# Kernel optimization log

Measured on AMD Instinct MI355X. Metric: run time of the kernel, lower is better.

The kernel has to match this reference:

```python
import jax, jax.numpy as jnp
import numpy as np


def setup_inputs() -> dict:
    key = jax.random.key(0)
    ks = jax.random.split(key, 5)
    B, S, D, H, dk = 4, 2048, 1024, 16, 64
    s = 0.02
    return {
        "x": jax.random.normal(ks[0], (B, S, D), dtype=jnp.float32),
        "Wq": jax.random.normal(ks[1], (H, D, dk), dtype=jnp.float32) * s,
        "Wk": jax.random.normal(ks[2], (H, D, dk), dtype=jnp.float32) * s,
        "Wv": jax.random.normal(ks[3], (H, D, dk), dtype=jnp.float32) * s,
        "Wo": jax.random.normal(ks[4], (H * dk, D), dtype=jnp.float32) * s,
    }


def reference(x, Wq, Wk, Wv, Wo):
    # Per-head projections: [B,S,D] x [H,D,dk] -> [B,H,S,dk]
    Q = jnp.einsum("bsd,hdk->bhsk", x, Wq)
    K = jnp.einsum("bsd,hdk->bhsk", x, Wk)
    V = jnp.einsum("bsd,hdk->bhsk", x, Wv)
    scale = 1.0 / jnp.sqrt(jnp.asarray(Wq.shape[-1], x.dtype))
    scores = jnp.einsum("bhqk,bhsk->bhqs", Q, K) * scale  # [B,H,S,S]
    attn = jax.nn.softmax(scores, axis=-1)
    out = jnp.einsum("bhqs,bhsk->bhqk", attn, V)  # [B,H,S,dk]
    B, H, S, dk = out.shape
    # concat heads along feature dim (matches torch.cat over head outputs)
    out = out.transpose(0, 2, 1, 3).reshape(B, S, H * dk)
    return out @ Wo  # [B,S,D]
```

## Files before the change

kernel.cpp:

```cpp
#include <hip/hip_runtime.h>
#include <hip/hip_bf16.h>
#include <stdint.h>

typedef __attribute__((ext_vector_type(8))) short bf16x8;
typedef __attribute__((ext_vector_type(4))) float f32x4;
typedef __attribute__((ext_vector_type(4))) unsigned short us4;

#define AS1C(p) ((const __attribute__((address_space(1))) void*)(p))
#define AS3(p)  ((__attribute__((address_space(3))) void*)(p))

#if __has_builtin(__builtin_amdgcn_exp2f)
#define EXP2(x) __builtin_amdgcn_exp2f(x)
#else
#define EXP2(x) __expf((x) * 0.69314718f)
#endif

#define MAX3(a,b,c) fmaxf(fmaxf((a),(b)),(c))

static __device__ __forceinline__ unsigned short f2b(float f) {
  union { __hip_bfloat16 h; unsigned short u; } cv;
  cv.h = __float2bfloat16(f);
  return cv.u;
}

static __device__ __forceinline__ unsigned int cvtpk(float a, float b) {
  unsigned int r;
  asm("v_cvt_pk_bf16_f32 %0, %1, %2" : "=v"(r) : "v"(a), "v"(b));
  return r;
}

__global__ __launch_bounds__(256) void conv_x_kernel(const float* __restrict__ x,
                                                     unsigned short* __restrict__ xb,
                                                     int n4) {
  int i = blockIdx.x * 256 + threadIdx.x;
  if (i >= n4) return;
  float4 v = ((const float4*)x)[i];
  us4 r = { f2b(v.x), f2b(v.y), f2b(v.z), f2b(v.w) };
  *(us4*)&xb[(size_t)i * 4] = r;
}

__global__ __launch_bounds__(256) void conv_wqkv_kernel(const float* __restrict__ Wq,
                                                        const float* __restrict__ Wk,
                                                        const float* __restrict__ Wv,
                                                        unsigned short* __restrict__ WqkvT) {
  int bid = blockIdx.x;
  int which = bid >> 8;
  int h  = (bid >> 4) & 15;
  int dt = bid & 15;
  const float* W = (which == 0) ? Wq : (which == 1 ? Wk : Wv);
  __shared__ float tile[64][65];
  const int t = threadIdx.x;
  const int c  = t & 63;
  const int r0 = t >> 6;
  const float* src = W + (size_t)h * 65536 + (size_t)dt * 64 * 64;
#pragma unroll
  for (int it = 0; it < 16; ++it) {
    int r = r0 + it * 4;
    tile[r][c] = src[r * 64 + c];
  }
  __syncthreads();
  const size_t n0 = (size_t)which * 1024 + h * 64;
  const int d0 = dt * 64;
#pragma unroll
  for (int it = 0; it < 16; ++it) {
    int cc = r0 + it * 4;
    WqkvT[(n0 + cc) * 1024 + d0 + c] = f2b(tile[c][cc]);
  }
}

__global__ __launch_bounds__(256) void conv_wo_kernel(const float* __restrict__ Wo,
                                                      unsigned short* __restrict__ WoT) {
  int kt = blockIdx.x >> 4, nt = blockIdx.x & 15;
  __shared__ float tile[64][65];
  const int t = threadIdx.x;
  const int c  = t & 63;
  const int r0 = t >> 6;
  const float* src = Wo + (size_t)(kt * 64) * 1024 + nt * 64;
#pragma unroll
  for (int it = 0; it < 16; ++it) {
    int r = r0 + it * 4;
    tile[r][c] = src[(size_t)r * 1024 + c];
  }
  __syncthreads();
#pragma unroll
  for (int it = 0; it < 16; ++it) {
    int cc = r0 + it * 4;
    WoT[((size_t)nt * 64 + cc) * 1024 + kt * 64 + c] = f2b(tile[c][cc]);
  }
}

__global__ __launch_bounds__(256) void gemm_qkv_kernel(
    const unsigned short* __restrict__ A,
    const unsigned short* __restrict__ Bt,
    unsigned short* __restrict__ Q,
    unsigned short* __restrict__ Ko,
    unsigned short* __restrict__ Vt) {
  __shared__ __align__(16) unsigned short sA[128 * 32];
  __shared__ __align__(16) unsigned short sB[128 * 32];
  const int tid  = threadIdx.x;
  const int lane = tid & 63;
  const int wid  = tid >> 6;
  const int wr = wid >> 1, wc = wid & 1;
  const int n0 = blockIdx.y * 24 + blockIdx.x;
  const int n1 = (n0 & 7) * 192 + (n0 >> 3);
  const int brow = (n1 / 24) * 128;
  const int bcol = (n1 % 24) * 128;
  const int K = 1024;

  f32x4 acc[4][4] = {};

  const int r4 = tid >> 2;
  const int c8 = (tid & 3) * 8;
  const unsigned short* ga = A  + (size_t)(brow + r4) * K + c8;
  const unsigned short* gb = Bt + (size_t)(bcol + r4) * K + c8;
  unsigned short* lAw = sA + wid * 512;
  unsigned short* lBw = sB + wid * 512;

  for (int kb = 0; kb < K; kb += 32) {
    if (kb) __syncthreads();
    __builtin_amdgcn_global_load_lds(AS1C(ga + kb),            AS3(lAw),        16, 0, 0);
    __builtin_amdgcn_global_load_lds(AS1C(ga + 64 * K + kb),   AS3(lAw + 2048), 16, 0, 0);
    __builtin_amdgcn_global_load_lds(AS1C(gb + kb),            AS3(lBw),        16, 0, 0);
    __builtin_amdgcn_global_load_lds(AS1C(gb + 64 * K + kb),   AS3(lBw + 2048), 16, 0, 0);
    __syncthreads();

    bf16x8 af[4], bfr[4];
#pragma unroll
    for (int mi = 0; mi < 4; ++mi)
      af[mi] = *(const bf16x8*)&sA[(wr * 64 + mi * 16 + (lane & 15)) * 32 + (lane >> 4) * 8];
#pragma unroll
    for (int ni = 0; ni < 4; ++ni)
      bfr[ni] = *(const bf16x8*)&sB[(wc * 64 + ni * 16 + (lane & 15)) * 32 + (lane >> 4) * 8];
#pragma unroll
    for (int mi = 0; mi < 4; ++mi)
#pragma unroll
      for (int ni = 0; ni < 4; ++ni)
        acc[mi][ni] = __builtin_amdgcn_mfma_f32_16x16x32_bf16(af[mi], bfr[ni], acc[mi][ni], 0, 0, 0);
  }

#pragma unroll
  for (int mi = 0; mi < 4; ++mi) {
    int row0 = brow + wr * 64 + mi * 16 + (lane >> 4) * 4;
    int b = row0 >> 11, s0 = row0 & 2047;
#pragma unroll
    for (int ni = 0; ni < 4; ++ni) {
      int col = bcol + wc * 64 + ni * 16 + (lane & 15);
      int which = col >> 10;
      int h  = (col >> 6) & 15;
      int kk = col & 63;
      if (which == 2) {
        us4 pk = { f2b(acc[mi][ni][0]), f2b(acc[mi][ni][1]),
                   f2b(acc[mi][ni][2]), f2b(acc[mi][ni][3]) };
        *(us4*)&Vt[((size_t)(b * 16 + h) * 64 + kk) * 2048 + s0] = pk;
      } else {
        unsigned short* dst = (which == 0) ? Q : Ko;
        float scl = (which == 0) ? 0.18033688f : 1.0f;
#pragma unroll
        for (int j = 0; j < 4; ++j)
          dst[((size_t)(b * 16 + h) * 2048 + (s0 + j)) * 64 + kk] = f2b(acc[mi][ni][j] * scl);
      }
    }
  }
}

__global__ __launch_bounds__(256) void gemm_out_kernel(
    const unsigned short* __restrict__ A,
    const unsigned short* __restrict__ Bt,
    float* __restrict__ out) {
  __shared__ __align__(16) unsigned short sA[128 * 32];
  __shared__ __align__(16) unsigned short sB[128 * 32];
  const int tid  = threadIdx.x;
  const int lane = tid & 63;
  const int wid  = tid >> 6;
  const int wr = wid >> 1, wc = wid & 1;
  const int n0 = blockIdx.y * 8 + blockIdx.x;
  const int n1 = (n0 & 7) * 64 + (n0 >> 3);
  const int brow = (n1 >> 3) * 128;
  const int bcol = (n1 & 7) * 128;
  const int K = 1024;

  f32x4 acc[4][4] = {};

  const int r4 = tid >> 2;
  const int c8 = (tid & 3) * 8;
  const unsigned short* ga = A  + (size_t)(brow + r4) * K + c8;
  const unsigned short* gb = Bt + (size_t)(bcol + r4) * K + c8;
  unsigned short* lAw = sA + wid * 512;
  unsigned short* lBw = sB + wid * 512;

  for (int kb = 0; kb < K; kb += 32) {
    if (kb) __syncthreads();
    __builtin_amdgcn_global_load_lds(AS1C(ga + kb),          AS3(lAw),        16, 0, 0);
    __builtin_amdgcn_global_load_lds(AS1C(ga + 64 * K + kb), AS3(lAw + 2048), 16, 0, 0);
    __builtin_amdgcn_global_load_lds(AS1C(gb + kb),          AS3(lBw),        16, 0, 0);
    __builtin_amdgcn_global_load_lds(AS1C(gb + 64 * K + kb), AS3(lBw + 2048), 16, 0, 0);
    __syncthreads();

    bf16x8 af[4], bfr[4];
#pragma unroll
    for (int mi = 0; mi < 4; ++mi)
      af[mi] = *(const bf16x8*)&sA[(wr * 64 + mi * 16 + (lane & 15)) * 32 + (lane >> 4) * 8];
#pragma unroll
    for (int ni = 0; ni < 4; ++ni)
      bfr[ni] = *(const bf16x8*)&sB[(wc * 64 + ni * 16 + (lane & 15)) * 32 + (lane >> 4) * 8];
#pragma unroll
    for (int mi = 0; mi < 4; ++mi)
#pragma unroll
      for (int ni = 0; ni < 4; ++ni)
        acc[mi][ni] = __builtin_amdgcn_mfma_f32_16x16x32_bf16(af[mi], bfr[ni], acc[mi][ni], 0, 0, 0);
  }

#pragma unroll
  for (int mi = 0; mi < 4; ++mi) {
    int row0 = brow + wr * 64 + mi * 16 + (lane >> 4) * 4;
#pragma unroll
    for (int ni = 0; ni < 4; ++ni) {
      int col = bcol + wc * 64 + ni * 16 + (lane & 15);
#pragma unroll
      for (int j = 0; j < 4; ++j)
        out[(size_t)(row0 + j) * 1024 + col] = acc[mi][ni][j];
    }
  }
}

__global__ __launch_bounds__(512) void attn_kernel(
    const unsigned short* __restrict__ Q,
    const unsigned short* __restrict__ K,
    const unsigned short* __restrict__ Vt,
    unsigned short* __restrict__ O) {
  __shared__ __align__(16) unsigned short sK[2][64 * 64];
  __shared__ __align__(16) unsigned short sVt[2][64 * 64];
  __shared__ __align__(16) unsigned short sP[16][16 * 72];

  const int tid = threadIdx.x, lane = tid & 63, w = tid >> 6;
  const int l15 = lane & 15, hi = lane >> 4;
  const int n = blockIdx.x + (blockIdx.y << 3);
  const int bh = (n & 7) * 8 + (n >> 6);
  const int qx = (n >> 3) & 7;
  const int qb = qx * 256;
  const unsigned short* Qp  = Q  + (size_t)bh * 131072;
  const unsigned short* Kp  = K  + (size_t)bh * 131072;
  const unsigned short* Vtp = Vt + (size_t)bh * 131072;

  bf16x8 qf[2][2];
#pragma unroll
  for (int mi = 0; mi < 2; ++mi) {
    int qrow = qb + w * 32 + mi * 16 + l15;
    qf[mi][0] = *(const bf16x8*)&Qp[(size_t)qrow * 64 + hi * 8];
    qf[mi][1] = *(const bf16x8*)&Qp[(size_t)qrow * 64 + 32 + hi * 8];
  }

  f32x4 o[2][4] = {};
  float m_[2] = { 0.f, 0.f };
  float l_[2] = { 0.f, 0.f };

  const int lrow = lane >> 3;
  const int uch  = (lane & 7) ^ lrow;
  const unsigned short* kg = Kp  + (size_t)(w * 8 + lrow) * 64   + uch * 8;
  const unsigned short* vg = Vtp + (size_t)(w * 8 + lrow) * 2048 + uch * 8;
  unsigned short* dK0 = &sK[0][w * 512];
  unsigned short* dK1 = &sK[1][w * 512];
  unsigned short* dV0 = &sVt[0][w * 512];
  unsigned short* dV1 = &sVt[1][w * 512];

  const int x7 = l15 & 7;
  const int ck0 = (hi ^ x7) * 8;
  const int ck1 = ((hi + 4) ^ x7) * 8;

  __builtin_amdgcn_global_load_lds(AS1C(kg), AS3(dK0), 16, 0, 0);
  __builtin_amdgcn_global_load_lds(AS1C(vg), AS3(dV0), 16, 0, 0);
  __syncthreads();

  for (int kt = 0; kt < 32; ++kt) {
    const int cur = kt & 1;
    if (kt < 31) {
      kg += 4096; vg += 64;
      __builtin_amdgcn_global_load_lds(AS1C(kg), AS3(cur ? dK0 : dK1), 16, 0, 0);
      __builtin_amdgcn_global_load_lds(AS1C(vg), AS3(cur ? dV0 : dV1), 16, 0, 0);
    }
    const unsigned short* sKc  = &sK[cur][0];
    const unsigned short* sVtc = &sVt[cur][0];

#pragma unroll
    for (int mi = 0; mi < 2; ++mi) {
      f32x4 sc[4] = {};
      __builtin_amdgcn_s_setprio(1);
#pragma unroll
      for (int ni = 0; ni < 4; ++ni) {
        bf16x8 kf0 = *(const bf16x8*)&sKc[(ni * 16 + l15) * 64 + ck0];
        bf16x8 kf1 = *(const bf16x8*)&sKc[(ni * 16 + l15) * 64 + ck1];
        sc[ni] = __builtin_amdgcn_mfma_f32_16x16x32_bf16(kf0, qf[mi][0], sc[ni], 0, 0, 0);
        sc[ni] = __builtin_amdgcn_mfma_f32_16x16x32_bf16(kf1, qf[mi][1], sc[ni], 0, 0, 0);
      }
      __builtin_amdgcn_s_setprio(0);

      float t0 = MAX3(sc[0][0], sc[0][1], sc[0][2]);
      float t1 = MAX3(sc[0][3], sc[1][0], sc[1][1]);
      float t2 = MAX3(sc[1][2], sc[1][3], sc[2][0]);
      float t3 = MAX3(sc[2][1], sc[2][2], sc[2][3]);
      float t4 = MAX3(sc[3][0], sc[3][1], sc[3][2]);
      float pmax = fmaxf(MAX3(t0, t1, t2), MAX3(t3, t4, sc[3][3]));

      if (!__all(pmax - m_[mi] <= 8.0f)) {
        pmax = fmaxf(pmax, __shfl_xor(pmax, 16));
        pmax = fmaxf(pmax, __shfl_xor(pmax, 32));
        float mnew  = fmaxf(m_[mi], pmax);
        float alpha = EXP2(m_[mi] - mnew);
        l_[mi] *= alpha;
#pragma unroll
        for (int j = 0; j < 4; ++j) {
          float aj = __shfl(alpha, hi * 4 + j);
#pragma unroll
          for (int ni = 0; ni < 4; ++ni) o[mi][ni][j] *= aj;
        }
        m_[mi] = mnew;
      }

      const float mcur = m_[mi];
      f32x4 sum4 = {};
#pragma unroll
      for (int ni = 0; ni < 4; ++ni)
#pragma unroll
        for (int r = 0; r < 4; ++r) {
          float p = EXP2(sc[ni][r] - mcur);
          sc[ni][r] = p;
          sum4[r] += p;
        }
      l_[mi] += (sum4[0] + sum4[1]) + (sum4[2] + sum4[3]);

      unsigned short* pb = &sP[w * 2 + mi][l15 * 72];
#pragma unroll
      for (int ni = 0; ni < 4; ++ni) {
        uint2 pk = { cvtpk(sc[ni][0], sc[ni][1]), cvtpk(sc[ni][2], sc[ni][3]) };
        *(uint2*)&pb[ni * 16 + hi * 4] = pk;
      }
    }

    bf16x8 pa[2][2];
#pragma unroll
    for (int mi = 0; mi < 2; ++mi) {
      pa[mi][0] = *(const bf16x8*)&sP[w * 2 + mi][l15 * 72 + hi * 8];
      pa[mi][1] = *(const bf16x8*)&sP[w * 2 + mi][l15 * 72 + 32 + hi * 8];
    }
    __builtin_amdgcn_s_setprio(1);
#pragma unroll
    for (int ni = 0; ni < 4; ++ni) {
      bf16x8 vf0 = *(const bf16x8*)&sVtc[(ni * 16 + l15) * 64 + ck0];
      bf16x8 vf1 = *(const bf16x8*)&sVtc[(ni * 16 + l15) * 64 + ck1];
#pragma unroll
      for (int mi = 0; mi < 2; ++mi) {
        o[mi][ni] = __builtin_amdgcn_mfma_f32_16x16x32_bf16(pa[mi][0], vf0, o[mi][ni], 0, 0, 0);
        o[mi][ni] = __builtin_amdgcn_mfma_f32_16x16x32_bf16(pa[mi][1], vf1, o[mi][ni], 0, 0, 0);
      }
    }
    __builtin_amdgcn_s_setprio(0);

    __syncthreads();
  }

  const int b = bh >> 4, h = bh & 15;
#pragma unroll
  for (int mi = 0; mi < 2; ++mi) {
    float lm = l_[mi];
    lm += __shfl_xor(lm, 16);
    lm += __shfl_xor(lm, 32);
    float linv = 1.0f / lm;
#pragma unroll
    for (int j = 0; j < 4; ++j) {
      float inv = __shfl(linv, hi * 4 + j);
      int row = qb + w * 32 + mi * 16 + hi * 4 + j;
#pragma unroll
      for (int ni = 0; ni < 4; ++ni)
        O[((size_t)b * 2048 + row) * 1024 + h * 64 + ni * 16 + l15] = f2b(o[mi][ni][j] * inv);
    }
  }
}

extern "C" void kernel_launch(void* const* d_in, const int* in_sizes, int n_in,
                              void* d_out, int out_size, void* d_ws, size_t ws_size,
                              hipStream_t stream) {
  const float* x  = (const float*)d_in[0];
  const float* Wq = (const float*)d_in[1];
  const float* Wk = (const float*)d_in[2];
  const float* Wv = (const float*)d_in[3];
  const float* Wo = (const float*)d_in[4];
  float* out = (float*)d_out;

  char* w = (char*)d_ws;
  unsigned short* xb   = (unsigned short*)(w);
  unsigned short* wqkv = (unsigned short*)(w + 16777216);
  unsigned short* wo   = (unsigned short*)(w + 23068672);
  unsigned short* Qb   = (unsigned short*)(w + 25165824);
  unsigned short* Kb   = (unsigned short*)(w + 41943040);
  unsigned short* Vtb  = (unsigned short*)(w + 58720256);
  unsigned short* Ob   = (unsigned short*)(w + 75497472);

  conv_x_kernel<<<8192, 256, 0, stream>>>(x, xb, 2097152);
  conv_wqkv_kernel<<<768, 256, 0, stream>>>(Wq, Wk, Wv, wqkv);
  conv_wo_kernel<<<256, 256, 0, stream>>>(Wo, wo);
  gemm_qkv_kernel<<<dim3(24, 64), 256, 0, stream>>>(xb, wqkv, Qb, Kb, Vtb);
  attn_kernel<<<dim3(8, 64), 512, 0, stream>>>(Qb, Kb, Vtb, Ob);
  gemm_out_kernel<<<dim3(8, 64), 256, 0, stream>>>(Ob, wo, out);
}
```

Measured before the change: 190.7 us.

## Fold max subtraction into MFMA accumulator init and compute row sums via MFMA

Starts the QK^T accumulators at -m so the MFMA itself yields the max-shifted scores, removing a per-element subtract before exp2. The softmax denominator is now accumulated by MFMA against a vector of bf16 ones, replacing scalar per-element adds and the final cross-lane shuffle reduction. The row sum is therefore taken from bf16-rounded probabilities, matching what the PV product uses. The cost is extra MFMA work per tile, plus a rescale path that now subtracts delta from every score.

After: 184.6 us. -3.2%, faster.

```diff
diff --git a/kernel.cpp b/kernel.cpp
--- a/kernel.cpp
+++ b/kernel.cpp
@@ -250,9 +250,13 @@
     qf[mi][1] = *(const bf16x8*)&Qp[(size_t)qrow * 64 + 32 + hi * 8];
   }
 
+  bf16x8 ones;
+#pragma unroll
+  for (int j = 0; j < 8; ++j) ones[j] = (short)0x3F80;
+
   f32x4 o[2][4] = {};
+  f32x4 lacc[2] = {};
   float m_[2] = { 0.f, 0.f };
-  float l_[2] = { 0.f, 0.f };
 
   const int lrow = lane >> 3;
   const int uch  = (lane & 7) ^ lrow;
@@ -283,7 +287,9 @@
 
 #pragma unroll
     for (int mi = 0; mi < 2; ++mi) {
-      f32x4 sc[4] = {};
+      const float mneg = -m_[mi];
+      f32x4 sc[4] = { { mneg, mneg, mneg, mneg }, { mneg, mneg, mneg, mneg },
+                      { mneg, mneg, mneg, mneg }, { mneg, mneg, mneg, mneg } };
       __builtin_amdgcn_s_setprio(1);
 #pragma unroll
       for (int ni = 0; ni < 4; ++ni) {
@@ -301,37 +307,38 @@
       float t4 = MAX3(sc[3][0], sc[3][1], sc[3][2]);
       float pmax = fmaxf(MAX3(t0, t1, t2), MAX3(t3, t4, sc[3][3]));
 
-      if (!__all(pmax - m_[mi] <= 8.0f)) {
+      if (!__all(pmax <= 8.0f)) {
         pmax = fmaxf(pmax, __shfl_xor(pmax, 16));
         pmax = fmaxf(pmax, __shfl_xor(pmax, 32));
-        float mnew  = fmaxf(m_[mi], pmax);
-        float alpha = EXP2(m_[mi] - mnew);
-        l_[mi] *= alpha;
+        float delta = fmaxf(pmax, 0.f);
+        float alpha = EXP2(-delta);
 #pragma unroll
         for (int j = 0; j < 4; ++j) {
-          float aj = __shfl(alpha, hi * 4 + j);
+          float dj = __shfl(delta, hi * 4 + j);
+          float aj = EXP2(-dj);
+          lacc[mi][j] *= aj;
 #pragma unroll
           for (int ni = 0; ni < 4; ++ni) o[mi][ni][j] *= aj;
         }
-        m_[mi] = mnew;
+#pragma unroll
+        for (int ni = 0; ni < 4; ++ni)
+#pragma unroll
+          for (int r = 0; r < 4; ++r) sc[ni][r] -= delta;
+        m_[mi] += delta;
+        (void)alpha;
       }
 
-      const float mcur = m_[mi];
-      f32x4 sum4 = {};
+      f32x4 p4[4];
 #pragma unroll
       for (int ni = 0; ni < 4; ++ni)
 #pragma unroll
-        for (int r = 0; r < 4; ++r) {
-          float p = EXP2(sc[ni][r] - mcur);
-          sc[ni][r] = p;
-          sum4[r] += p;
-        }
-      l_[mi] += (sum4[0] + sum4[1]) + (sum4[2] + sum4[3]);
+        for (int r = 0; r < 4; ++r)
+          p4[ni][r] = EXP2(sc[ni][r]);
 
       unsigned short* pb = &sP[w * 2 + mi][l15 * 72];
 #pragma unroll
       for (int ni = 0; ni < 4; ++ni) {
-        uint2 pk = { cvtpk(sc[ni][0], sc[ni][1]), cvtpk(sc[ni][2], sc[ni][3]) };
+        uint2 pk = { cvtpk(p4[ni][0], p4[ni][1]), cvtpk(p4[ni][2], p4[ni][3]) };
         *(uint2*)&pb[ni * 16 + hi * 4] = pk;
       }
     }
@@ -343,6 +350,11 @@
       pa[mi][1] = *(const bf16x8*)&sP[w * 2 + mi][l15 * 72 + 32 + hi * 8];
     }
     __builtin_amdgcn_s_setprio(1);
+#pragma unroll
+    for (int mi = 0; mi < 2; ++mi) {
+      lacc[mi] = __builtin_amdgcn_mfma_f32_16x16x32_bf16(pa[mi][0], ones, lacc[mi], 0, 0, 0);
+      lacc[mi] = __builtin_amdgcn_mfma_f32_16x16x32_bf16(pa[mi][1], ones, lacc[mi], 0, 0, 0);
+    }
 #pragma unroll
     for (int ni = 0; ni < 4; ++ni) {
       bf16x8 vf0 = *(const bf16x8*)&sVtc[(ni * 16 + l15) * 64 + ck0];
@@ -361,13 +373,9 @@
   const int b = bh >> 4, h = bh & 15;
 #pragma unroll
   for (int mi = 0; mi < 2; ++mi) {
-    float lm = l_[mi];
-    lm += __shfl_xor(lm, 16);
-    lm += __shfl_xor(lm, 32);
-    float linv = 1.0f / lm;
 #pragma unroll
     for (int j = 0; j < 4; ++j) {
-      float inv = __shfl(linv, hi * 4 + j);
+      float inv = 1.0f / lacc[mi][j];
       int row = qb + w * 32 + mi * 16 + hi * 4 + j;
 #pragma unroll
       for (int ni = 0; ni < 4; ++ni)
```
